# Optimization experiments

Measured on AMD Instinct MI355X. Metric: run time of the kernel, lower is better.

Reference implementation:

```python
import math
import jax, jax.numpy as jnp
import numpy as np

V = 32000   # vocab_size
NL = 8      # n_layer
NH = 16     # n_head
D = 1024    # n_embd
DH = D // NH
FF = 4 * D
B = 2
L = 1024
EPS = 1e-5


def setup_inputs() -> dict:
    key = jax.random.key(0)
    ks = jax.random.split(key, 10)
    std = 0.02  # matches nn.init.normal_(std=0.02)
    def nrm(k, shape):
        return jax.random.normal(k, shape, jnp.float32) * std
    return {
        "idx": jax.random.randint(ks[0], (B, L), 0, V),
        "tok_emb": nrm(ks[1], (V, D)),
        # per-layer params stacked on leading NL axis (scanned over)
        "ln1_w": jnp.ones((NL, D)), "ln1_b": jnp.zeros((NL, D)),
        "wq": nrm(ks[2], (NL, D, D)), "wk": nrm(ks[3], (NL, D, D)),
        "wv": nrm(ks[4], (NL, D, D)), "wo": nrm(ks[5], (NL, D, D)),
        "ln2_w": jnp.ones((NL, D)), "ln2_b": jnp.zeros((NL, D)),
        "w1": nrm(ks[6], (NL, D, FF)), "b1": jnp.zeros((NL, FF)),
        "w2": nrm(ks[7], (NL, FF, D)), "b2": jnp.zeros((NL, D)),
        "lnf_w": jnp.ones((D,)), "lnf_b": jnp.zeros((D,)),
        "lm_head": nrm(ks[8], (D, V)),
    }


def _sinusoidal_pe(seq_len, dim):
    pos = jnp.arange(seq_len, dtype=jnp.float32)[:, None]
    div = jnp.exp(jnp.arange(0, dim, 2, dtype=jnp.float32) * (-math.log(10000.0) / dim))
    pe = jnp.zeros((seq_len, dim), jnp.float32)
    pe = pe.at[:, 0::2].set(jnp.sin(pos * div))
    pe = pe.at[:, 1::2].set(jnp.cos(pos * div))
    return pe


def _ln(x, w, b):
    m = x.mean(-1, keepdims=True)
    v = ((x - m) ** 2).mean(-1, keepdims=True)
    return (x - m) * jax.lax.rsqrt(v + EPS) * w + b


def reference(idx, tok_emb, ln1_w, ln1_b, wq, wk, wv, wo,
              ln2_w, ln2_b, w1, b1, w2, b2, lnf_w, lnf_b, lm_head):
    b, l = idx.shape
    x = tok_emb[idx] + _sinusoidal_pe(l, tok_emb.shape[1])[None]  # [B,L,D]
    causal = jnp.tril(jnp.ones((l, l), bool))
    scale = 1.0 / math.sqrt(DH)

    def block(x, p):
        l1w, l1b, Wq, Wk, Wv, Wo, l2w, l2b, W1, B1, W2, B2 = p
        h = _ln(x, l1w, l1b)
        def heads(W):  # [B,L,D] -> [B,H,L,DH]
            return (h @ W).reshape(b, l, NH, DH).transpose(0, 2, 1, 3)
        q, k, v = heads(Wq), heads(Wk), heads(Wv)
        att = jnp.einsum('bhqd,bhkd->bhqk', q, k) * scale
        att = jnp.where(causal, att, -jnp.inf)
        att = jax.nn.softmax(att, axis=-1)
        y = jnp.einsum('bhqk,bhkd->bhqd', att, v)
        y = y.transpose(0, 2, 1, 3).reshape(b, l, -1)
        x = x + y @ Wo
        h2 = _ln(x, l2w, l2b)
        x = x + jax.nn.gelu(h2 @ W1 + B1, approximate=False) @ W2 + B2
        return x, None

    x, _ = jax.lax.scan(
        block, x, (ln1_w, ln1_b, wq, wk, wv, wo, ln2_w, ln2_b, w1, b1, w2, b2))
    x = _ln(x, lnf_w, lnf_b)
    return x @ lm_head  # [B,L,V] logits
```

## Files before the change

### kernel.cpp

```cpp
#include <hip/hip_runtime.h>
#include <math.h>

typedef unsigned short u16;
typedef __bf16 bfx8 __attribute__((ext_vector_type(8)));
typedef float f32x4 __attribute__((ext_vector_type(4)));

#define NLAYER  8
#define NHEAD   16
#define DMODEL  1024
#define DHEAD   64
#define DFF     4096
#define NB      2
#define SEQ     1024
#define NVOCAB  32000
#define NTOK    (NB*SEQ)
#define EPSLN   1e-5f
#define VCHUNK  6400
#define NSPLIT  2

__device__ __forceinline__ float bf2f(u16 u) {
  union { unsigned int i; float f; } x; x.i = ((unsigned int)u) << 16; return x.f;
}
__device__ __forceinline__ u16 f2bf(float f) {
  unsigned int x = __float_as_uint(f);
  x += 0x7fffu + ((x >> 16) & 1u);
  return (u16)(x >> 16);
}

#if defined(__has_builtin)
#if __has_builtin(__builtin_amdgcn_global_load_lds)
#define HAVE_GLL 1
#endif
#endif

__device__ __forceinline__ void gll16(const void* g, void* lds_base, int lane) {
#ifdef HAVE_GLL
  __builtin_amdgcn_global_load_lds((const __attribute__((address_space(1))) unsigned int*)g,
                                   (__attribute__((address_space(3))) unsigned int*)lds_base,
                                   16, 0, 0);
  (void)lane;
#else
  *(uint4*)((char*)lds_base + lane * 16) = *(const uint4*)g;
#endif
}

enum { EPI_QKV = 0, EPI_GELU_BIAS = 1, EPI_RESID = 2, EPI_RESID_BIAS = 3, EPI_LOGITS = 4 };

template <int EPI, int BM>
__global__ __launch_bounds__(256) void gemm_bt(
    const u16* __restrict__ A, const u16* __restrict__ Bt,
    const float* __restrict__ bias, u16* __restrict__ outb,
    float* __restrict__ outf, int M, int N, int K, int ldc)
{
  constexpr int ARND = BM / 32;
  constexpr int MF = BM / 32;
  constexpr int ABYTES = BM * 64 * 2;
  constexpr int BBYTES = 128 * 64 * 2;
  __shared__ __align__(16) u16 sA[2][BM * 64];
  __shared__ __align__(16) u16 sB[2][128 * 64];

  const int tid  = threadIdx.x;
  const int w    = tid >> 6;
  const int lane = tid & 63;
  const int l16  = lane & 15;
  const int hi   = lane >> 4;
  const int wm   = w >> 1;
  const int wn   = w & 1;

  const int nwg = gridDim.x;
  const int MB  = M / BM;
  const int orig = blockIdx.x;
  const int xcd = orig & 7, li = orig >> 3;
  const int q = nwg >> 3, r = nwg & 7;
  const int work = (xcd < r ? xcd * (q + 1) : r * (q + 1) + (xcd - r) * q) + li;
  const int m0 = (work % MB) * BM;
  const int n0 = (work / MB) * 128;

  const int srow8 = lane >> 3;
  const int su    = lane & 7;

  const u16* gA[ARND]; const u16* gB[4];
  int laOff[ARND]; int lbOff[4];
#pragma unroll
  for (int r2 = 0; r2 < ARND; r2++) {
    const int row = r2 * 32 + w * 8 + srow8;
    const int gu = su ^ (row & 7);
    gA[r2] = A + (size_t)(m0 + row) * K + gu * 8;
    laOff[r2] = (r2 * 32 + w * 8) * 128;
  }
#pragma unroll
  for (int r2 = 0; r2 < 4; r2++) {
    const int row = r2 * 32 + w * 8 + srow8;
    const int gu = su ^ (row & 7);
    gB[r2] = Bt + (size_t)(n0 + row) * K + gu * 8;
    lbOff[r2] = (r2 * 32 + w * 8) * 128;
  }

  f32x4 acc[MF][4];
#pragma unroll
  for (int i = 0; i < MF; i++)
#pragma unroll
    for (int j = 0; j < 4; j++)
#pragma unroll
      for (int r2 = 0; r2 < 4; r2++) acc[i][j][r2] = 0.0f;

#pragma unroll
  for (int r2 = 0; r2 < ARND; r2++) { gll16(gA[r2], (char*)sA[0] + laOff[r2], lane); gA[r2] += 64; }
#pragma unroll
  for (int r2 = 0; r2 < 4; r2++)    { gll16(gB[r2], (char*)sB[0] + lbOff[r2], lane); gB[r2] += 64; }
  __syncthreads();

  const int NT = K >> 6;
  int cur = 0;
  for (int t = 0; t < NT; ++t) {
    if (t + 1 < NT) {
      char* nA = (char*)sA[0] + (cur ^ 1) * ABYTES;
      char* nB = (char*)sB[0] + (cur ^ 1) * BBYTES;
#pragma unroll
      for (int r2 = 0; r2 < ARND; r2++) { gll16(gA[r2], nA + laOff[r2], lane); gA[r2] += 64; }
#pragma unroll
      for (int r2 = 0; r2 < 4; r2++)    { gll16(gB[r2], nB + lbOff[r2], lane); gB[r2] += 64; }
    }

    const char* cA = (const char*)sA[0] + cur * ABYTES;
    const char* cB = (const char*)sB[0] + cur * BBYTES;
    bfx8 aF[MF][2], bF[4][2];
#pragma unroll
    for (int i = 0; i < MF; i++) {
      const int row = wm * (BM / 2) + i * 16 + l16;
      const int rsw = row & 7;
#pragma unroll
      for (int kk = 0; kk < 2; kk++)
        aF[i][kk] = *(const bfx8*)(cA + row * 128 + ((kk * 4 + hi) ^ rsw) * 16);
    }
#pragma unroll
    for (int j = 0; j < 4; j++) {
      const int row = wn * 64 + j * 16 + l16;
      const int rsw = row & 7;
#pragma unroll
      for (int kk = 0; kk < 2; kk++)
        bF[j][kk] = *(const bfx8*)(cB + row * 128 + ((kk * 4 + hi) ^ rsw) * 16);
    }
#pragma unroll
    for (int kk = 0; kk < 2; kk++)
#pragma unroll
      for (int i = 0; i < MF; i++)
#pragma unroll
        for (int j = 0; j < 4; j++)
          acc[i][j] = __builtin_amdgcn_mfma_f32_16x16x32_bf16(aF[i][kk], bF[j][kk], acc[i][j], 0, 0, 0);
    __syncthreads();
    cur ^= 1;
  }

  const int rbase = m0 + wm * (BM / 2);
  const int cbase = n0 + wn * 64;
#pragma unroll
  for (int i = 0; i < MF; i++) {
#pragma unroll
    for (int j = 0; j < 4; j++) {
      const int gcol = cbase + j * 16 + l16;
      float bv = 0.0f;
      if constexpr (EPI == EPI_GELU_BIAS || EPI == EPI_RESID_BIAS) bv = bias[gcol];
#pragma unroll
      for (int r2 = 0; r2 < 4; r2++) {
        const int grow = rbase + i * 16 + hi * 4 + r2;
        float v = acc[i][j][r2];
        const size_t oi = (size_t)grow * ldc + gcol;
        if constexpr (EPI == EPI_QKV) {
          outb[oi] = f2bf(v);
        } else if constexpr (EPI == EPI_GELU_BIAS) {
          v += bv;
          v = 0.5f * v * (1.0f + erff(v * 0.70710678118654752f));
          outb[oi] = f2bf(v);
        } else if constexpr (EPI == EPI_RESID) {
          outf[oi] += v;
        } else if constexpr (EPI == EPI_RESID_BIAS) {
          outf[oi] += v + bv;
        } else {
          outf[oi] = v;
        }
      }
    }
  }
}

__global__ __launch_bounds__(256) void ln_kernel(
    const float* __restrict__ x, const float* __restrict__ w,
    const float* __restrict__ b, u16* __restrict__ out)
{
  const int row = blockIdx.x;
  const int tid = threadIdx.x;
  const float* xr = x + (size_t)row * DMODEL;
  float4 v = *(const float4*)(xr + tid * 4);
  __shared__ float sbuf[4];
  float s = v.x + v.y + v.z + v.w;
#pragma unroll
  for (int o = 32; o > 0; o >>= 1) s += __shfl_xor(s, o, 64);
  if ((tid & 63) == 0) sbuf[tid >> 6] = s;
  __syncthreads();
  const float mean = (sbuf[0] + sbuf[1] + sbuf[2] + sbuf[3]) * (1.0f / DMODEL);
  __syncthreads();
  float d0 = v.x - mean, d1 = v.y - mean, d2 = v.z - mean, d3 = v.w - mean;
  float qq = d0 * d0 + d1 * d1 + d2 * d2 + d3 * d3;
#pragma unroll
  for (int o = 32; o > 0; o >>= 1) qq += __shfl_xor(qq, o, 64);
  if ((tid & 63) == 0) sbuf[tid >> 6] = qq;
  __syncthreads();
  const float var = (sbuf[0] + sbuf[1] + sbuf[2] + sbuf[3]) * (1.0f / DMODEL);
  const float rstd = rsqrtf(var + EPSLN);
  const int c = tid * 4;
  float dv[4] = {d0, d1, d2, d3};
#pragma unroll
  for (int e = 0; e < 4; e++)
    out[(size_t)row * DMODEL + c + e] = f2bf(dv[e] * rstd * w[c + e] + b[c + e]);
}

__global__ __launch_bounds__(256) void embed_kernel(
    const int* __restrict__ idx, const float* __restrict__ tok, float* __restrict__ x)
{
  const int row = blockIdx.x;
  const int l = row & (SEQ - 1);
  const int t = idx[row];
  const int d = threadIdx.x * 4;
#pragma unroll
  for (int e = 0; e < 4; e++) {
    const int dd = d + e;
    const float freq = expf((float)(dd & ~1) * (-9.210340371976184f / (float)DMODEL));
    const float ang = (float)l * freq;
    const float pe = (dd & 1) ? cosf(ang) : sinf(ang);
    x[(size_t)row * DMODEL + dd] = tok[(size_t)t * DMODEL + dd] + pe;
  }
}

__global__ __launch_bounds__(256) void transpose_b(
    const float* __restrict__ in0, u16* __restrict__ out0, int rows, int cols,
    size_t in_ls, size_t out_ls)
{
  __shared__ float tile[32][33];
  const float* in = in0 + (size_t)blockIdx.z * in_ls;
  u16* out = out0 + (size_t)blockIdx.z * out_ls;
  const int c0 = blockIdx.x * 32, r0 = blockIdx.y * 32;
  const int tx = threadIdx.x & 31, ty = threadIdx.x >> 5;
#pragma unroll
  for (int i = ty; i < 32; i += 8)
    tile[i][tx] = in[(size_t)(r0 + i) * cols + c0 + tx];
  __syncthreads();
#pragma unroll
  for (int i = ty; i < 32; i += 8)
    out[(size_t)(c0 + i) * rows + r0 + tx] = f2bf(tile[tx][i]);
}

__global__ __launch_bounds__(256) void transpose6_kernel(
    const float* __restrict__ wq, const float* __restrict__ wk,
    const float* __restrict__ wv, const float* __restrict__ wo,
    const float* __restrict__ w1, const float* __restrict__ w2,
    u16* __restrict__ wT)
{
  __shared__ float tile[32][33];
  const size_t dd = (size_t)DMODEL * DMODEL, dff = (size_t)DMODEL * DFF;
  const int t = blockIdx.x;
  const float* in; u16* out; int rows, cols, cx, cy;
  if (t < 4096) {
    const int mat = t >> 10, tl = t & 1023;
    in = (mat == 0) ? wq : (mat == 1) ? wk : (mat == 2) ? wv : wo;
    out = wT + (size_t)mat * dd; rows = DMODEL; cols = DMODEL;
    cx = tl & 31; cy = tl >> 5;
  } else if (t < 8192) {
    const int tl = t - 4096;
    in = w1; out = wT + 4 * dd; rows = DMODEL; cols = DFF;
    cx = tl & 127; cy = tl >> 7;
  } else {
    const int tl = t - 8192;
    in = w2; out = wT + 4 * dd + dff; rows = DFF; cols = DMODEL;
    cx = tl & 31; cy = tl >> 5;
  }
  const int c0 = cx * 32, r0 = cy * 32;
  const int tx = threadIdx.x & 31, ty = threadIdx.x >> 5;
#pragma unroll
  for (int i = ty; i < 32; i += 8)
    tile[i][tx] = in[(size_t)(r0 + i) * cols + c0 + tx];
  __syncthreads();
#pragma unroll
  for (int i = ty; i < 32; i += 8)
    out[(size_t)(c0 + i) * rows + r0 + tx] = f2bf(tile[tx][i]);
}

__global__ __launch_bounds__(256) void vtrans_kernel(
    const u16* __restrict__ qkv, u16* __restrict__ vt)
{
  __shared__ u16 tile[32][33];
  const int bh = blockIdx.z;
  const int b = bh >> 4, hh = bh & 15;
  const int l0 = blockIdx.x * 32, d0 = blockIdx.y * 32;
  const int tx = threadIdx.x & 31, ty = threadIdx.x >> 5;
#pragma unroll
  for (int i = ty; i < 32; i += 8)
    tile[i][tx] = qkv[(size_t)(b * SEQ + l0 + i) * (3 * DMODEL) + 2 * DMODEL + hh * DHEAD + d0 + tx];
  __syncthreads();
#pragma unroll
  for (int i = ty; i < 32; i += 8)
    vt[(size_t)(bh * DHEAD + d0 + i) * SEQ + l0 + tx] = tile[tx][i];
}

__device__ __forceinline__ int plds_byte(int row, int col) {
  return row * 128 + ((((col >> 3) ^ (row & 7)) << 3) + (col & 7)) * 2;
}

__global__ __launch_bounds__(64) void attn_partial(
    const u16* __restrict__ qkv, const u16* __restrict__ vt,
    float* __restrict__ opart, float* __restrict__ lpart)
{
  __shared__ __align__(16) u16 p_lds[32 * 64];
  const int lane = threadIdx.x;
  const int l16 = lane & 15, hi = lane >> 4;
  const int qt = blockIdx.x, hh = blockIdx.y;
  const int b = blockIdx.z >> 1, sp = blockIdx.z & 1;
  const int q0 = qt * 32;
  const int T = (q0 + 95) >> 6;
  const int t_lo = (T * sp) >> 1;
  const int t_hi = (T * (sp + 1)) >> 1;

  const u16* qptr = qkv;
  const u16* kptr = qkv + DMODEL;
  const size_t rs3 = 3 * DMODEL;
  const size_t hoff = (size_t)hh * DHEAD;

  bfx8 aQ[2][2];
#pragma unroll
  for (int mt = 0; mt < 2; mt++)
#pragma unroll
    for (int kf = 0; kf < 2; kf++)
      aQ[mt][kf] = *(const bfx8*)&qptr[(size_t)(b * SEQ + q0 + mt * 16 + l16) * rs3 + hoff + kf * 32 + hi * 8];

  f32x4 o[2][4];
  float ssum[2][4];
#pragma unroll
  for (int mt = 0; mt < 2; mt++)
#pragma unroll
    for (int r = 0; r < 4; r++) ssum[mt][r] = 0.0f;
#pragma unroll
  for (int mt = 0; mt < 2; mt++)
#pragma unroll
    for (int dt = 0; dt < 4; dt++)
#pragma unroll
      for (int r = 0; r < 4; r++) o[mt][dt][r] = 0.0f;

  for (int kt = t_lo; kt < t_hi; kt++) {
    const int k0 = kt * 64;
    const bool diag = (kt == T - 1);

    bfx8 bK[4][2];
#pragma unroll
    for (int nt = 0; nt < 4; nt++)
#pragma unroll
      for (int kf = 0; kf < 2; kf++)
        bK[nt][kf] = *(const bfx8*)&kptr[(size_t)(b * SEQ + k0 + nt * 16 + l16) * rs3 + hoff + kf * 32 + hi * 8];

    f32x4 s[2][4];
#pragma unroll
    for (int mt = 0; mt < 2; mt++)
#pragma unroll
      for (int nt = 0; nt < 4; nt++) {
#pragma unroll
        for (int r = 0; r < 4; r++) s[mt][nt][r] = 0.0f;
        s[mt][nt] = __builtin_amdgcn_mfma_f32_16x16x32_bf16(aQ[mt][0], bK[nt][0], s[mt][nt], 0, 0, 0);
        s[mt][nt] = __builtin_amdgcn_mfma_f32_16x16x32_bf16(aQ[mt][1], bK[nt][1], s[mt][nt], 0, 0, 0);
      }

#pragma unroll
    for (int mt = 0; mt < 2; mt++) {
#pragma unroll
      for (int r = 0; r < 4; r++) {
        const int row_l = mt * 16 + hi * 4 + r;
        const int qrow = q0 + row_l;
        float p[4], rsum = 0.0f;
#pragma unroll
        for (int nt = 0; nt < 4; nt++) {
          const float sv = s[mt][nt][r] * 0.125f;
          const bool mask = diag && (k0 + nt * 16 + l16 > qrow);
          p[nt] = mask ? 0.0f : __expf(sv);
          rsum += p[nt];
        }
#pragma unroll
        for (int t = 1; t < 16; t <<= 1) rsum += __shfl_xor(rsum, t, 64);
        ssum[mt][r] += rsum;
#pragma unroll
        for (int nt = 0; nt < 4; nt++)
          *(u16*)((char*)p_lds + plds_byte(row_l, nt * 16 + l16)) = f2bf(p[nt]);
      }
    }
    __syncthreads();

    bfx8 pa[2][2];
#pragma unroll
    for (int mt = 0; mt < 2; mt++) {
      const int row = mt * 16 + l16;
#pragma unroll
      for (int kf = 0; kf < 2; kf++)
        pa[mt][kf] = *(const bfx8*)((const char*)p_lds + row * 128 + (((kf * 4 + hi) ^ (row & 7)) << 4));
    }
    bfx8 bV[4][2];
    const size_t vbase = (size_t)(b * NHEAD + hh) * DHEAD * SEQ;
#pragma unroll
    for (int dt = 0; dt < 4; dt++)
#pragma unroll
      for (int kf = 0; kf < 2; kf++)
        bV[dt][kf] = *(const bfx8*)&vt[vbase + (size_t)(dt * 16 + l16) * SEQ + k0 + kf * 32 + hi * 8];
#pragma unroll
    for (int mt = 0; mt < 2; mt++)
#pragma unroll
      for (int dt = 0; dt < 4; dt++) {
        o[mt][dt] = __builtin_amdgcn_mfma_f32_16x16x32_bf16(pa[mt][0], bV[dt][0], o[mt][dt], 0, 0, 0);
        o[mt][dt] = __builtin_amdgcn_mfma_f32_16x16x32_bf16(pa[mt][1], bV[dt][1], o[mt][dt], 0, 0, 0);
      }
    __syncthreads();
  }

  const size_t pbase = (((size_t)sp * NB + b) * NHEAD + hh) * SEQ + q0;
#pragma unroll
  for (int mt = 0; mt < 2; mt++) {
#pragma unroll
    for (int r = 0; r < 4; r++) {
      const int row_l = mt * 16 + hi * 4 + r;
      const size_t rg = pbase + row_l;
      if (l16 == 0) lpart[rg] = ssum[mt][r];
#pragma unroll
      for (int dt = 0; dt < 4; dt++)
        opart[rg * DHEAD + dt * 16 + l16] = o[mt][dt][r];
    }
  }
}

__global__ __launch_bounds__(256) void attn_combine(
    const float* __restrict__ opart, const float* __restrict__ lpart,
    u16* __restrict__ y)
{
  const int row = blockIdx.x;
  const int b = row >> 10;
  const int l = row & (SEQ - 1);
  const int t = threadIdx.x;
  const int hh = t >> 4;
  const int d0 = (t & 15) * 4;
  const size_t base = ((size_t)b * NHEAD + hh) * SEQ + l;
  const size_t stride = (size_t)NB * NHEAD * SEQ;
  float wsum = 0.0f;
  float4 acc = make_float4(0.f, 0.f, 0.f, 0.f);
#pragma unroll
  for (int i = 0; i < NSPLIT; i++) {
    wsum += lpart[base + i * stride];
    const float4 ov = *(const float4*)&opart[(base + i * stride) * DHEAD + d0];
    acc.x += ov.x; acc.y += ov.y; acc.z += ov.z; acc.w += ov.w;
  }
  const float dn = 1.0f / wsum;
  u16* yp = y + (size_t)row * DMODEL + hh * DHEAD + d0;
  yp[0] = f2bf(acc.x * dn);
  yp[1] = f2bf(acc.y * dn);
  yp[2] = f2bf(acc.z * dn);
  yp[3] = f2bf(acc.w * dn);
}

extern "C" void kernel_launch(void* const* d_in, const int* in_sizes, int n_in,
                              void* d_out, int out_size, void* d_ws, size_t ws_size,
                              hipStream_t stream)
{
  (void)in_sizes; (void)n_in; (void)out_size;
  const int*   idx  = (const int*)d_in[0];
  const float* tok  = (const float*)d_in[1];
  const float* ln1w = (const float*)d_in[2];
  const float* ln1b = (const float*)d_in[3];
  const float* wq   = (const float*)d_in[4];
  const float* wk   = (const float*)d_in[5];
  const float* wv   = (const float*)d_in[6];
  const float* wo   = (const float*)d_in[7];
  const float* ln2w = (const float*)d_in[8];
  const float* ln2b = (const float*)d_in[9];
  const float* w1   = (const float*)d_in[10];
  const float* b1   = (const float*)d_in[11];
  const float* w2   = (const float*)d_in[12];
  const float* b2   = (const float*)d_in[13];
  const float* lnfw = (const float*)d_in[14];
  const float* lnfb = (const float*)d_in[15];
  const float* lmh  = (const float*)d_in[16];
  float* out = (float*)d_out;

  char* ws = (char*)d_ws;
  size_t off = 0;
  auto alloc = [&](size_t bytes) -> void* {
    void* p = ws + off;
    off += (bytes + 255) & ~(size_t)255;
    return p;
  };
  float* x  = (float*)alloc((size_t)NTOK * DMODEL * 4);
  u16* h    = (u16*)alloc((size_t)NTOK * DMODEL * 2);
  u16* qkv  = (u16*)alloc((size_t)NTOK * 3 * DMODEL * 2);
  u16* vtb  = (u16*)alloc((size_t)NTOK * DMODEL * 2);
  u16* yb   = (u16*)alloc((size_t)NTOK * DMODEL * 2);
  u16* ffb  = (u16*)alloc((size_t)NTOK * DFF * 2);
  float* opart = (float*)alloc((size_t)NSPLIT * NB * NHEAD * SEQ * DHEAD * 4);
  float* lpart = (float*)alloc((size_t)NSPLIT * NB * NHEAD * SEQ * 4);

  const size_t dd = (size_t)DMODEL * DMODEL, dff = (size_t)DMODEL * DFF;
  const size_t perLayerElems = 4 * dd + 2 * dff;
  const size_t wT_bytes = perLayerElems * 2;
  const size_t lmhT_bytes = (size_t)NVOCAB * DMODEL * 2;

  u16* wT = (u16*)alloc(wT_bytes);
  const bool full_lmh = (off + lmhT_bytes) <= ws_size;
  u16* lmhT = full_lmh ? (u16*)alloc(lmhT_bytes) : nullptr;

  embed_kernel<<<NTOK, 256, 0, stream>>>(idx, tok, x);

  const int gQKV = (3 * DMODEL / 128) * (NTOK / 128);
  const int gFF1 = (DFF / 128) * (NTOK / 128);
  const int gD64 = (DMODEL / 128) * (NTOK / 64);

  u16* wqT = wT;
  u16* woT = wT + 3 * dd;
  u16* w1T = wT + 4 * dd;
  u16* w2T = w1T + dff;

  for (int layer = 0; layer < NLAYER; layer++) {
    transpose6_kernel<<<12288, 256, 0, stream>>>(
        wq + layer * dd, wk + layer * dd, wv + layer * dd, wo + layer * dd,
        w1 + layer * dff, w2 + layer * dff, wT);

    ln_kernel<<<NTOK, 256, 0, stream>>>(x, ln1w + layer * DMODEL, ln1b + layer * DMODEL, h);
    gemm_bt<EPI_QKV, 128><<<gQKV, 256, 0, stream>>>(h, wqT, nullptr, qkv, nullptr,
                                                    NTOK, 3 * DMODEL, DMODEL, 3 * DMODEL);
    vtrans_kernel<<<dim3(SEQ / 32, DHEAD / 32, NB * NHEAD), 256, 0, stream>>>(qkv, vtb);
    attn_partial<<<dim3(SEQ / 32, NHEAD, NB * NSPLIT), 64, 0, stream>>>(
        qkv, vtb, opart, lpart);
    attn_combine<<<NB * SEQ, 256, 0, stream>>>(opart, lpart, yb);
    gemm_bt<EPI_RESID, 64><<<gD64, 256, 0, stream>>>(yb, woT, nullptr, nullptr, x,
                                                     NTOK, DMODEL, DMODEL, DMODEL);
    ln_kernel<<<NTOK, 256, 0, stream>>>(x, ln2w + layer * DMODEL, ln2b + layer * DMODEL, h);
    gemm_bt<EPI_GELU_BIAS, 128><<<gFF1, 256, 0, stream>>>(h, w1T, b1 + (size_t)layer * DFF, ffb,
                                                          nullptr, NTOK, DFF, DMODEL, DFF);
    gemm_bt<EPI_RESID_BIAS, 64><<<gD64, 256, 0, stream>>>(ffb, w2T, b2 + (size_t)layer * DMODEL,
                                                          nullptr, x, NTOK, DMODEL, DFF, DMODEL);
  }

  ln_kernel<<<NTOK, 256, 0, stream>>>(x, lnfw, lnfb, h);

  if (full_lmh) {
    transpose_b<<<dim3(NVOCAB/32, DMODEL/32, 1), 256, 0, stream>>>(lmh, lmhT, DMODEL, NVOCAB, 0, 0);
    const int gLM = (NVOCAB / 128) * (NTOK / 128);
    gemm_bt<EPI_LOGITS, 128><<<gLM, 256, 0, stream>>>(
        h, lmhT, nullptr, nullptr, out, NTOK, NVOCAB, DMODEL, NVOCAB);
  } else {
    for (int c = 0; c < NVOCAB / VCHUNK; c++) {
      transpose_b<<<dim3(VCHUNK/32, DMODEL/32, 1), 256, 0, stream>>>(
          lmh + (size_t)c * VCHUNK, wT, DMODEL, NVOCAB, 0, 0);
      gemm_bt<EPI_LOGITS, 128><<<(VCHUNK / 128) * (NTOK / 128), 256, 0, stream>>>(
          h, wT, nullptr, nullptr, out + (size_t)c * VCHUNK,
          NTOK, VCHUNK, DMODEL, NVOCAB);
    }
  }
}
```

Before: 1.915 ms.

## Add 8-wave 128x256 triple-buffered GEMM for QKV, FF1 and LM head

Adds a new 512-thread GEMM kernel with a 128x256 output tile. It triple-buffers global-to-LDS loads, spreading them across the four MFMA sub-steps, and raises wave priority around the MFMA blocks. Work items are remapped per XCD so neighbouring tiles share L2. It replaces the 256-thread 128x128 kernel for the QKV, FF1-GELU and logits GEMMs, aiming at more data reuse per block and better overlap of memory and compute. The trade-off is 144KB of LDS per block and fewer blocks, e.g. 192 for QKV on a 256-CU device, which may underfill the GPU.

```diff
diff --git a/kernel.cpp b/kernel.cpp
--- a/kernel.cpp
+++ b/kernel.cpp
@@ -45,6 +45,169 @@
 }
 
 enum { EPI_QKV = 0, EPI_GELU_BIAS = 1, EPI_RESID = 2, EPI_RESID_BIAS = 3, EPI_LOGITS = 4 };
+
+__device__ __forceinline__ void epi_store(int EPI_, float v, float bv,
+                                          u16* outb, float* outf, size_t oi) {
+  (void)EPI_; (void)v; (void)bv; (void)outb; (void)outf; (void)oi;
+}
+
+template <int EPI>
+__global__ __launch_bounds__(512) void gemm_bt8(
+    const u16* __restrict__ A, const u16* __restrict__ Bt,
+    const float* __restrict__ bias, u16* __restrict__ outb,
+    float* __restrict__ outf, int M, int N, int K, int ldc)
+{
+  __shared__ __align__(16) u16 sA[3][128 * 64];
+  __shared__ __align__(16) u16 sB[3][256 * 64];
+
+  const int tid  = threadIdx.x;
+  const int w    = tid >> 6;
+  const int lane = tid & 63;
+  const int l16  = lane & 15;
+  const int hi   = lane >> 4;
+  const int wm   = w >> 2;
+  const int wn   = w & 3;
+
+  const int nwg = gridDim.x;
+  const int MB  = M / 128;
+  const int orig = blockIdx.x;
+  const int xcd = orig & 7, li = orig >> 3;
+  const int q_ = nwg >> 3, r_ = nwg & 7;
+  const int work = (xcd < r_ ? xcd * (q_ + 1) : r_ * (q_ + 1) + (xcd - r_) * q_) + li;
+  const int m0 = (work % MB) * 128;
+  const int n0 = (work / MB) * 256;
+
+  const int srow = tid >> 3;
+  const int su   = tid & 7;
+
+  const u16* gA[2]; const u16* gB[4];
+  int laOff[2], lbOff[4];
+#pragma unroll
+  for (int r = 0; r < 2; r++) {
+    const int row = r * 64 + srow;
+    gA[r] = A + (size_t)(m0 + row) * K + (size_t)((su ^ (row & 7)) * 8);
+    laOff[r] = (r * 64 + w * 8) * 128;
+  }
+#pragma unroll
+  for (int r = 0; r < 4; r++) {
+    const int row = r * 64 + srow;
+    gB[r] = Bt + (size_t)(n0 + row) * K + (size_t)((su ^ (row & 7)) * 8);
+    lbOff[r] = (r * 64 + w * 8) * 128;
+  }
+
+  f32x4 acc[4][4];
+#pragma unroll
+  for (int i = 0; i < 4; i++)
+#pragma unroll
+    for (int j = 0; j < 4; j++)
+#pragma unroll
+      for (int r2 = 0; r2 < 4; r2++) acc[i][j][r2] = 0.0f;
+
+  const int NT = K >> 6;
+
+#pragma unroll
+  for (int r = 0; r < 2; r++) { gll16(gA[r], (char*)sA[0] + laOff[r], lane); gA[r] += 64; }
+#pragma unroll
+  for (int r = 0; r < 4; r++) { gll16(gB[r], (char*)sB[0] + lbOff[r], lane); gB[r] += 64; }
+#pragma unroll
+  for (int r = 0; r < 2; r++) { gll16(gA[r], (char*)sA[1] + laOff[r], lane); gA[r] += 64; }
+#pragma unroll
+  for (int r = 0; r < 4; r++) { gll16(gB[r], (char*)sB[1] + lbOff[r], lane); gB[r] += 64; }
+  asm volatile("s_waitcnt vmcnt(6)" ::: "memory");
+  __builtin_amdgcn_sched_barrier(0);
+  __builtin_amdgcn_s_barrier();
+
+  int cbuf = 0;
+  for (int t = 0; t < NT; ++t) {
+    const int nbuf = (cbuf + 2 >= 3) ? (cbuf - 1) : (cbuf + 2);
+    const bool stg = (t + 2 < NT);
+    const char* cA = (const char*)sA[cbuf];
+    const char* cB = (const char*)sB[cbuf];
+    char* nA = (char*)sA[nbuf];
+    char* nB = (char*)sB[nbuf];
+
+#pragma unroll
+    for (int q = 0; q < 4; ++q) {
+      const int i0 = (q >> 1) * 2;
+      const int j0 = (q & 1) * 2;
+      bfx8 aF[2][2], bF[2][2];
+#pragma unroll
+      for (int ii = 0; ii < 2; ii++) {
+        const int row = wm * 64 + (i0 + ii) * 16 + l16;
+        const int rsw = row & 7;
+#pragma unroll
+        for (int kk = 0; kk < 2; kk++)
+          aF[ii][kk] = *(const bfx8*)(cA + row * 128 + ((kk * 4 + hi) ^ rsw) * 16);
+      }
+#pragma unroll
+      for (int jj = 0; jj < 2; jj++) {
+        const int row = wn * 64 + (j0 + jj) * 16 + l16;
+        const int rsw = row & 7;
+#pragma unroll
+        for (int kk = 0; kk < 2; kk++)
+          bF[jj][kk] = *(const bfx8*)(cB + row * 128 + ((kk * 4 + hi) ^ rsw) * 16);
+      }
+      if (stg) {
+        if (q == 0) {
+          gll16(gA[0], nA + laOff[0], lane); gA[0] += 64;
+          gll16(gA[1], nA + laOff[1], lane); gA[1] += 64;
+        } else if (q == 1) {
+          gll16(gB[0], nB + lbOff[0], lane); gB[0] += 64;
+          gll16(gB[1], nB + lbOff[1], lane); gB[1] += 64;
+        } else if (q == 2) {
+          gll16(gB[2], nB + lbOff[2], lane); gB[2] += 64;
+        } else {
+          gll16(gB[3], nB + lbOff[3], lane); gB[3] += 64;
+        }
+      }
+      __builtin_amdgcn_s_barrier();
+      __builtin_amdgcn_s_setprio(1);
+#pragma unroll
+      for (int kk = 0; kk < 2; kk++)
+#pragma unroll
+        for (int ii = 0; ii < 2; ii++)
+#pragma unroll
+          for (int jj = 0; jj < 2; jj++)
+            acc[i0 + ii][j0 + jj] = __builtin_amdgcn_mfma_f32_16x16x32_bf16(
+                aF[ii][kk], bF[jj][kk], acc[i0 + ii][j0 + jj], 0, 0, 0);
+      __builtin_amdgcn_s_setprio(0);
+      __builtin_amdgcn_s_barrier();
+    }
+
+    if (t < NT - 2) { asm volatile("s_waitcnt vmcnt(6)" ::: "memory"); }
+    else            { asm volatile("s_waitcnt vmcnt(0)" ::: "memory"); }
+    __builtin_amdgcn_sched_barrier(0);
+    __builtin_amdgcn_s_barrier();
+    cbuf = (cbuf + 1 == 3) ? 0 : cbuf + 1;
+  }
+
+  const int rbase = m0 + wm * 64;
+  const int cbase = n0 + wn * 64;
+#pragma unroll
+  for (int i = 0; i < 4; i++) {
+#pragma unroll
+    for (int j = 0; j < 4; j++) {
+      const int gcol = cbase + j * 16 + l16;
+      float bv = 0.0f;
+      if constexpr (EPI == EPI_GELU_BIAS) bv = bias[gcol];
+#pragma unroll
+      for (int r2 = 0; r2 < 4; r2++) {
+        const int grow = rbase + i * 16 + hi * 4 + r2;
+        float v = acc[i][j][r2];
+        const size_t oi = (size_t)grow * ldc + gcol;
+        if constexpr (EPI == EPI_QKV) {
+          outb[oi] = f2bf(v);
+        } else if constexpr (EPI == EPI_GELU_BIAS) {
+          v += bv;
+          v = 0.5f * v * (1.0f + erff(v * 0.70710678118654752f));
+          outb[oi] = f2bf(v);
+        } else {
+          outf[oi] = v;
+        }
+      }
+    }
+  }
+}
 
 template <int EPI, int BM>
 __global__ __launch_bounds__(256) void gemm_bt(
@@ -510,9 +673,9 @@
 
   embed_kernel<<<NTOK, 256, 0, stream>>>(idx, tok, x);
 
-  const int gQKV = (3 * DMODEL / 128) * (NTOK / 128);
-  const int gFF1 = (DFF / 128) * (NTOK / 128);
-  const int gD64 = (DMODEL / 128) * (NTOK / 64);
+  const int gQKV8 = (NTOK / 128) * (3 * DMODEL / 256);
+  const int gFF18 = (NTOK / 128) * (DFF / 256);
+  const int gD64  = (DMODEL / 128) * (NTOK / 64);
 
   u16* wqT = wT;
   u16* woT = wT + 3 * dd;
@@ -525,8 +688,8 @@
         w1 + layer * dff, w2 + layer * dff, wT);
 
     ln_kernel<<<NTOK, 256, 0, stream>>>(x, ln1w + layer * DMODEL, ln1b + layer * DMODEL, h);
-    gemm_bt<EPI_QKV, 128><<<gQKV, 256, 0, stream>>>(h, wqT, nullptr, qkv, nullptr,
-                                                    NTOK, 3 * DMODEL, DMODEL, 3 * DMODEL);
+    gemm_bt8<EPI_QKV><<<gQKV8, 512, 0, stream>>>(h, wqT, nullptr, qkv, nullptr,
+                                                 NTOK, 3 * DMODEL, DMODEL, 3 * DMODEL);
     vtrans_kernel<<<dim3(SEQ / 32, DHEAD / 32, NB * NHEAD), 256, 0, stream>>>(qkv, vtb);
     attn_partial<<<dim3(SEQ / 32, NHEAD, NB * NSPLIT), 64, 0, stream>>>(
         qkv, vtb, opart, lpart);
@@ -534,8 +697,8 @@
     gemm_bt<EPI_RESID, 64><<<gD64, 256, 0, stream>>>(yb, woT, nullptr, nullptr, x,
                                                      NTOK, DMODEL, DMODEL, DMODEL);
     ln_kernel<<<NTOK, 256, 0, stream>>>(x, ln2w + layer * DMODEL, ln2b + layer * DMODEL, h);
-    gemm_bt<EPI_GELU_BIAS, 128><<<gFF1, 256, 0, stream>>>(h, w1T, b1 + (size_t)layer * DFF, ffb,
-                                                          nullptr, NTOK, DFF, DMODEL, DFF);
+    gemm_bt8<EPI_GELU_BIAS><<<gFF18, 512, 0, stream>>>(h, w1T, b1 + (size_t)layer * DFF, ffb,
+                                                       nullptr, NTOK, DFF, DMODEL, DFF);
     gemm_bt<EPI_RESID_BIAS, 64><<<gD64, 256, 0, stream>>>(ffb, w2T, b2 + (size_t)layer * DMODEL,
                                                           nullptr, x, NTOK, DMODEL, DFF, DMODEL);
   }
@@ -544,14 +707,14 @@
 
   if (full_lmh) {
     transpose_b<<<dim3(NVOCAB/32, DMODEL/32, 1), 256, 0, stream>>>(lmh, lmhT, DMODEL, NVOCAB, 0, 0);
-    const int gLM = (NVOCAB / 128) * (NTOK / 128);
-    gemm_bt<EPI_LOGITS, 128><<<gLM, 256, 0, stream>>>(
+    const int gLM8 = (NTOK / 128) * (NVOCAB / 256);
+    gemm_bt8<EPI_LOGITS><<<gLM8, 512, 0, stream>>>(
         h, lmhT, nullptr, nullptr, out, NTOK, NVOCAB, DMODEL, NVOCAB);
   } else {
     for (int c = 0; c < NVOCAB / VCHUNK; c++) {
       transpose_b<<<dim3(VCHUNK/32, DMODEL/32, 1), 256, 0, stream>>>(
           lmh + (size_t)c * VCHUNK, wT, DMODEL, NVOCAB, 0, 0);
-      gemm_bt<EPI_LOGITS, 128><<<(VCHUNK / 128) * (NTOK / 128), 256, 0, stream>>>(
+      gemm_bt8<EPI_LOGITS><<<(NTOK / 128) * (VCHUNK / 256), 512, 0, stream>>>(
           h, wT, nullptr, nullptr, out + (size_t)c * VCHUNK,
           NTOK, VCHUNK, DMODEL, NVOCAB);
     }
```

Measured after the change: 2.099 ms. +9.6%, slower.
